# Performance work log

Measured on AMD Instinct MI355X. Metric: run time of the kernel, lower is better.

## Reference

```python
import jax, jax.numpy as jnp
import numpy as np

L = 401            # cfg.n_anchor_bins
MIN_SEP = 2        # cfg.min_separation_bins
TARGET_ALPHA = 0.85
DIST_W, CTCF_W, COMP_W = 1.0, 0.5, 0.5
RATIO_TARGET = 1.5


def setup_inputs() -> dict:
    key = jax.random.key(0)
    k1, k2, k3 = jax.random.split(key, 3)
    B = 256
    contact_map = jax.random.normal(k1, (B, L, L), dtype=jnp.float32)
    compartment_logits = jax.random.normal(k2, (B, L, 2), dtype=jnp.float32)
    ctcf_orientation = (jax.random.randint(k3, (B, L), 0, 3) - 1).astype(jnp.int32)  # {-1,0,1}
    return {"contact_map": contact_map,
            "compartment_logits": compartment_logits,
            "ctcf_orientation": ctcf_orientation}


def reference(contact_map, compartment_logits, ctcf_orientation):
    B, Ld, _ = contact_map.shape
    dt = contact_map.dtype
    idx = jnp.arange(Ld)
    d = jnp.abs(idx[:, None] - idx[None, :])          # (L, L) int distance bins

    # ---- distance decay loss: one segment-reduce instead of a loop over bins ----
    bins = d.reshape(-1)                               # (L*L,)
    cm_sum = contact_map.sum(0).reshape(-1)            # sum over batch, flattened
    per_bin_sum = jax.ops.segment_sum(cm_sum, bins, num_segments=Ld)
    counts = jax.ops.segment_sum(jnp.ones_like(cm_sum), bins, num_segments=Ld)
    mean_c = per_bin_sum / (counts * B)                # mean contact per distance s
    s_vals = jnp.arange(Ld).astype(dt)
    valid = (idx >= MIN_SEP) & jnp.isfinite(mean_c) & (mean_c > 0)
    w = valid.astype(dt)
    n = w.sum()
    log_d = jnp.log(jnp.maximum(s_vals, 1.0))
    log_p = jnp.log(jnp.where(valid, mean_c, 1.0) + 1e-6)
    n_safe = jnp.maximum(n, 1.0)
    x_mean = (w * log_d).sum() / n_safe
    y_mean = (w * log_p).sum() / n_safe
    num = (w * (log_d - x_mean) * (log_p - y_mean)).sum()
    den = (w * (log_d - x_mean) ** 2).sum() + 1e-8
    slope = num / den
    dist_loss = jnp.where(n >= 5, (slope + TARGET_ALPHA) ** 2, jnp.zeros((), dt))

    # ---- CTCF convergence loss ----
    f = (ctcf_orientation == 1).astype(dt)             # (B, L)
    r = (ctcf_orientation == -1).astype(dt)
    convergent = f[:, :, None] * r[:, None, :]         # (B, L, L)
    any_c = (ctcf_orientation != 0).astype(dt)
    any_pair = any_c[:, :, None] * any_c[:, None, :]
    non_conv = any_pair * (1.0 - convergent)
    nc_sum = non_conv.sum()
    hinge = (jax.nn.relu(contact_map) * non_conv).sum() / (nc_sum + 1e-6)
    ctcf_loss = jnp.where(nc_sum < 1.0, jnp.zeros((), dt), hinge)

    # ---- compartment loss ----
    comp = jnp.argmax(jax.lax.stop_gradient(compartment_logits), axis=-1)  # (B, L)
    same = (comp[:, :, None] == comp[:, None, :]).astype(dt)               # (B, L, L)
    maskf = (d >= MIN_SEP).astype(dt)[None]                                # (1, L, L)
    within = (contact_map * same * maskf).sum() / jnp.maximum((same * maskf).sum(), 1.0)
    between = (contact_map * (1.0 - same) * maskf).sum() / jnp.maximum(((1.0 - same) * maskf).sum(), 1.0)
    ratio = within / (jnp.abs(between) + 1e-6)
    comp_loss = jax.nn.relu(RATIO_TARGET - ratio)

    total = DIST_W * dist_loss + CTCF_W * ctcf_loss + COMP_W * comp_loss
    return jnp.stack([dist_loss, ctcf_loss, comp_loss, total])
```

## Files before the change

kernel.cpp:

```cpp
#include <hip/hip_runtime.h>
#include <cmath>

#define LBINS 401
#define LL 160801
#define MIN_SEP 2
#define PSTRIDE 405
#define UNR 8

#define ACC_HANY  401
#define ACC_HCONV 402
#define ACC_SWM   403
#define ACC_SMM   404

__global__ __launch_bounds__(256)
void main_kernel(const float* __restrict__ cm,
                 const float* __restrict__ logits,
                 const int* __restrict__ ctcf,
                 float* __restrict__ parts,
                 int* __restrict__ partsI,
                 int* __restrict__ cnt) {
    int b      = blockIdx.x;
    int B      = gridDim.x;
    int ihalf  = blockIdx.y & 1;
    int kgroup = blockIdx.y >> 1;
    int u      = threadIdx.x;
    int k      = kgroup * 256 + u;
    bool active = (k < LBINS);

    __shared__ unsigned char colx8[LBINS];
    __shared__ __align__(8) unsigned char row8[LBINS + 7];
    __shared__ float lb[LBINS];
    __shared__ float sred[4][4];
    __shared__ int   ired[4][4];

    const int*   ct = ctcf   + (size_t)b * LBINS;
    const float* lg = logits + (size_t)b * LBINS * 2;
    for (int t = u; t < LBINS; t += 256) {
        int o = ct[t];
        unsigned any = (o != 0)  ? 1u : 0u;
        unsigned rev = (o == -1) ? 1u : 0u;
        unsigned fwd = (o == 1)  ? 1u : 0u;
        unsigned cj  = (lg[2 * t + 1] > lg[2 * t]) ? 1u : 0u;
        colx8[t] = (unsigned char)(any | (rev << 1) | (cj << 2));
        row8[t]  = (unsigned char)(any | (fwd << 1) | ((1u - cj) << 2));
        lb[t] = 0.f;
    }
    if (u < 7) row8[LBINS + u] = 0;
    if (b == 0 && blockIdx.y == 0 && u == 0)
        __hip_atomic_store(cnt, 0, __ATOMIC_RELAXED, __HIP_MEMORY_SCOPE_AGENT);
    __syncthreads();

    if (blockIdx.y == 0) {
        int na = 0, nr = 0, n1 = 0, adj = 0;
        for (int t = u; t < LBINS; t += 256) {
            unsigned cb = colx8[t];
            na += (int)(cb & 1u);
            nr += (int)((cb >> 1) & 1u);
            n1 += (int)((cb >> 2) & 1u);
            if (t >= 1) adj += (int)((((cb ^ colx8[t - 1]) >> 2) & 1u) ^ 1u);
        }
        #pragma unroll
        for (int off = 32; off > 0; off >>= 1) {
            na  += __shfl_down(na,  off, 64);
            nr  += __shfl_down(nr,  off, 64);
            n1  += __shfl_down(n1,  off, 64);
            adj += __shfl_down(adj, off, 64);
        }
        int w = u >> 6;
        if ((u & 63) == 0) {
            ired[w][0] = na; ired[w][1] = nr; ired[w][2] = n1; ired[w][3] = adj;
        }
        __syncthreads();
        if (u == 0) {
            int NA = ired[0][0] + ired[1][0] + ired[2][0] + ired[3][0];
            int NR = ired[0][1] + ired[1][1] + ired[2][1] + ired[3][1];
            int N1 = ired[0][2] + ired[1][2] + ired[2][2] + ired[3][2];
            int AD = ired[0][3] + ired[1][3] + ired[2][3] + ired[3][3];
            int NF = NA - NR;
            int N0 = LBINS - N1;
            partsI[b]     = NA * NA - NF * NR;
            partsI[B + b] = N0 * N0 + N1 * N1 - LBINS - 2 * AD;
        }
    }

    int i0 = ihalf ? 201 : 0;
    int ie = ihalf ? LBINS : 201;

    const float* cmb = cm + (size_t)b * LL;
    float HA = 0.f, HC = 0.f;
    float SMk = 0.f, SMw = 0.f, SWk = 0.f, SWw = 0.f;

    if (active) {
        auto scalar_step = [&](int ii) {
            int j = ii + k;
            int wrapped = (j >= LBINS);
            int jc = wrapped ? j - LBINS : j;
            float c = cmb[(size_t)ii * LBINS + jc];
            unsigned cbq = colx8[jc];
            unsigned rbq = row8[ii];
            float rc = fmaxf(c, 0.f);
            unsigned bnd = rbq & cbq;
            int m0 = (int)(bnd << 31) >> 31;
            int m1 = (int)(bnd << 30) >> 31;
            int ms = (int)((rbq ^ cbq) << 29) >> 31;
            HA += __int_as_float(__float_as_int(rc) & m0);
            HC += __int_as_float(__float_as_int(rc) & m1);
            float cs = __int_as_float(__float_as_int(c) & ms);
            SMw += wrapped ? c   : 0.f;
            SMk += wrapped ? 0.f : c;
            SWw += wrapped ? cs  : 0.f;
            SWk += wrapped ? 0.f : cs;
        };

        int i  = i0;
        int iu = i0 + ((8 - (i0 & 7)) & 7);
        if (iu > ie) iu = ie;
        for (; i < iu; ++i) scalar_step(i);
        for (; i + UNR <= ie; i += UNR) {
            unsigned long long rwin = *(const unsigned long long*)(row8 + i);
            float    cv[UNR];
            unsigned cb[UNR];
            int      wr[UNR];
            #pragma unroll
            for (int q = 0; q < UNR; ++q) {
                int ii = i + q;
                int j  = ii + k;
                int wrapped = (j >= LBINS);
                int jc = wrapped ? j - LBINS : j;
                cv[q] = cmb[(size_t)ii * LBINS + jc];
                cb[q] = colx8[jc];
                wr[q] = wrapped;
            }
            #pragma unroll
            for (int q = 0; q < UNR; ++q) {
                unsigned rbq = (unsigned)(rwin >> (8 * q)) & 0xffu;
                float c  = cv[q];
                float rc = fmaxf(c, 0.f);
                unsigned bnd = rbq & cb[q];
                int m0 = (int)(bnd << 31) >> 31;
                int m1 = (int)(bnd << 30) >> 31;
                int ms = (int)((rbq ^ cb[q]) << 29) >> 31;
                HA += __int_as_float(__float_as_int(rc) & m0);
                HC += __int_as_float(__float_as_int(rc) & m1);
                float cs = __int_as_float(__float_as_int(c) & ms);
                SMw += wr[q] ? c   : 0.f;
                SMk += wr[q] ? 0.f : c;
                SWw += wr[q] ? cs  : 0.f;
                SWk += wr[q] ? 0.f : cs;
            }
        }
        for (; i < ie; ++i) scalar_step(i);
    }

    float SWm = 0.f, SMm = 0.f;
    if (active) {
        int dw = LBINS - k;
        atomicAdd(&lb[k], SMk);
        if (k > 0) atomicAdd(&lb[dw], SMw);
        float mk = (k  >= MIN_SEP) ? 1.f : 0.f;
        float mw = (dw >= MIN_SEP) ? 1.f : 0.f;
        SWm = SWk * mk + SWw * mw;
        SMm = SMk * mk + SMw * mw;
    }

    #pragma unroll
    for (int off = 32; off > 0; off >>= 1) {
        HA  += __shfl_down(HA,  off, 64);
        HC  += __shfl_down(HC,  off, 64);
        SWm += __shfl_down(SWm, off, 64);
        SMm += __shfl_down(SMm, off, 64);
    }
    int w = u >> 6;
    if ((u & 63) == 0) {
        sred[w][0] = HA; sred[w][1] = HC; sred[w][2] = SWm; sred[w][3] = SMm;
    }
    __syncthreads();

    float* pout = parts + (size_t)(blockIdx.y * gridDim.x + blockIdx.x) * PSTRIDE;
    for (int t = u; t < LBINS; t += 256) pout[t] = lb[t];
    if (u == 0) {
        float a = 0.f, c2 = 0.f, s = 0.f, m = 0.f;
        #pragma unroll
        for (int q = 0; q < 4; ++q) {
            a += sred[q][0]; c2 += sred[q][1]; s += sred[q][2]; m += sred[q][3];
        }
        pout[ACC_HANY] = a; pout[ACC_HCONV] = c2;
        pout[ACC_SWM]  = s; pout[ACC_SMM]   = m;
    }
}

__device__ double br256(double v, double* buf) {
    int tid = threadIdx.x;
    buf[tid] = v;
    __syncthreads();
    for (int off = 128; off > 0; off >>= 1) {
        if (tid < off) buf[tid] += buf[tid + off];
        __syncthreads();
    }
    double r = buf[0];
    __syncthreads();
    return r;
}

__global__ __launch_bounds__(256)
void reduce_final_kernel(const float* __restrict__ parts,
                         const int* __restrict__ partsI,
                         float* __restrict__ accum,
                         int* __restrict__ accumI,
                         int* __restrict__ cnt,
                         float* __restrict__ out,
                         int B) {
    int s = blockIdx.x;
    int u = threadIdx.x;
    int npart = 4 * B;
    __shared__ float r4[4];
    __shared__ int   ri4[4];
    __shared__ int   lastFlag;

    if (s < PSTRIDE) {
        float acc = 0.f;
        for (int p = u; p < npart; p += 256) acc += parts[(size_t)p * PSTRIDE + s];
        #pragma unroll
        for (int off = 32; off > 0; off >>= 1) acc += __shfl_down(acc, off, 64);
        if ((u & 63) == 0) r4[u >> 6] = acc;
        __syncthreads();
        if (u == 0)
            __hip_atomic_store(&accum[s], r4[0] + r4[1] + r4[2] + r4[3],
                               __ATOMIC_RELAXED, __HIP_MEMORY_SCOPE_AGENT);
    } else {
        int col = s - PSTRIDE;
        int acc = 0;
        for (int p = u; p < B; p += 256) acc += partsI[col * B + p];
        #pragma unroll
        for (int off = 32; off > 0; off >>= 1) acc += __shfl_down(acc, off, 64);
        if ((u & 63) == 0) ri4[u >> 6] = acc;
        __syncthreads();
        if (u == 0)
            __hip_atomic_store(&accumI[col], ri4[0] + ri4[1] + ri4[2] + ri4[3],
                               __ATOMIC_RELAXED, __HIP_MEMORY_SCOPE_AGENT);
    }

    if (u == 0) {
        int prev = __hip_atomic_fetch_add(cnt, 1, __ATOMIC_ACQ_REL,
                                          __HIP_MEMORY_SCOPE_AGENT);
        lastFlag = (prev == (int)gridDim.x - 1);
    }
    __syncthreads();
    if (!lastFlag) return;

    __shared__ double dred[256];

    double nc_sum   = (double)__hip_atomic_load(&accumI[0], __ATOMIC_RELAXED,
                                                __HIP_MEMORY_SCOPE_AGENT);
    double same_cnt = (double)__hip_atomic_load(&accumI[1], __ATOMIC_RELAXED,
                                                __HIP_MEMORY_SCOPE_AGENT);
    double total_maskf = (double)B * ((double)LL - 3.0 * LBINS + 2.0);
    double diff_cnt = total_maskf - same_cnt;

    float w0 = 0.f, x0 = 0.f, y0 = 0.f;
    float w1 = 0.f, x1 = 0.f, y1 = 0.f;
    {
        int t0 = u;
        float a0 = __hip_atomic_load(&accum[t0], __ATOMIC_RELAXED,
                                     __HIP_MEMORY_SCOPE_AGENT);
        float cntB = ((t0 == 0) ? (float)LBINS : 2.0f * (float)(LBINS - t0)) * (float)B;
        float mc = a0 / cntB;
        int valid = (t0 >= MIN_SEP) && __builtin_isfinite(mc) && (mc > 0.0f);
        w0 = valid ? 1.f : 0.f;
        x0 = logf(fmaxf((float)t0, 1.0f));
        y0 = logf((valid ? mc : 1.0f) + 1e-6f);
    }
    int t1 = u + 256;
    if (t1 < LBINS) {
        float a1 = __hip_atomic_load(&accum[t1], __ATOMIC_RELAXED,
                                     __HIP_MEMORY_SCOPE_AGENT);
        float cntB = 2.0f * (float)(LBINS - t1) * (float)B;
        float mc = a1 / cntB;
        int valid = __builtin_isfinite(mc) && (mc > 0.0f);
        w1 = valid ? 1.f : 0.f;
        x1 = logf((float)t1);
        y1 = logf((valid ? mc : 1.0f) + 1e-6f);
    }
    double n  = br256((double)w0 + (double)w1, dred);
    double Sx = br256((double)(w0 * x0) + (double)(w1 * x1), dred);
    double Sy = br256((double)(w0 * y0) + (double)(w1 * y1), dred);
    double n_safe = fmax(n, 1.0);
    double xm = Sx / n_safe, ym = Sy / n_safe;
    double num = br256((double)w0 * ((double)x0 - xm) * ((double)y0 - ym)
                     + (double)w1 * ((double)x1 - xm) * ((double)y1 - ym), dred);
    double den = br256((double)w0 * ((double)x0 - xm) * ((double)x0 - xm)
                     + (double)w1 * ((double)x1 - xm) * ((double)x1 - xm), dred);

    if (u == 0) {
        double slope = num / (den + 1e-8);
        float dist_loss = (n >= 5.0) ? (float)((slope + 0.85) * (slope + 0.85)) : 0.0f;

        float fHA = __hip_atomic_load(&accum[ACC_HANY],  __ATOMIC_RELAXED, __HIP_MEMORY_SCOPE_AGENT);
        float fHC = __hip_atomic_load(&accum[ACC_HCONV], __ATOMIC_RELAXED, __HIP_MEMORY_SCOPE_AGENT);
        float fSW = __hip_atomic_load(&accum[ACC_SWM],   __ATOMIC_RELAXED, __HIP_MEMORY_SCOPE_AGENT);
        float fSM = __hip_atomic_load(&accum[ACC_SMM],   __ATOMIC_RELAXED, __HIP_MEMORY_SCOPE_AGENT);

        float ncf = (float)nc_sum;
        float hinge = (fHA - fHC) / (ncf + 1e-6f);
        float ctcf_loss = (ncf < 1.0f) ? 0.0f : hinge;

        float within  = fSW / (float)fmax(same_cnt, 1.0);
        float between = (fSM - fSW) / (float)fmax(diff_cnt, 1.0);
        float ratio = within / (fabsf(between) + 1e-6f);
        float comp_loss = fmaxf(1.5f - ratio, 0.0f);

        float total = 1.0f * dist_loss + 0.5f * ctcf_loss + 0.5f * comp_loss;
        out[0] = dist_loss;
        out[1] = ctcf_loss;
        out[2] = comp_loss;
        out[3] = total;
    }
}

extern "C" void kernel_launch(void* const* d_in, const int* in_sizes, int n_in,
                              void* d_out, int out_size, void* d_ws, size_t ws_size,
                              hipStream_t stream) {
    const float* cm     = (const float*)d_in[0];
    const float* logits = (const float*)d_in[1];
    const int*   ctcf   = (const int*)d_in[2];
    float* out = (float*)d_out;

    int total = in_sizes[0];
    int B = total / LL;

    float* wsf    = (float*)d_ws;
    float* accum  = wsf;
    int*   accumI = (int*)(wsf + 408);
    int*   cnt    = (int*)(wsf + 412);
    int*   partsI = (int*)(wsf + 416);
    int parts_off = (416 + 2 * B + 255) & ~255;
    float* parts  = wsf + parts_off;

    main_kernel<<<dim3(B, 4), 256, 0, stream>>>(cm, logits, ctcf, parts, partsI, cnt);
    reduce_final_kernel<<<PSTRIDE + 2, 256, 0, stream>>>(parts, partsI, accum,
                                                         accumI, cnt, out, B);
}
```

Measured before the change: 253.9 us.

## Split rows into three segments and double-buffer unrolled loads in main kernel

```diff
diff --git a/kernel.cpp b/kernel.cpp
--- a/kernel.cpp
+++ b/kernel.cpp
@@ -6,13 +6,15 @@
 #define MIN_SEP 2
 #define PSTRIDE 405
 #define UNR 8
+#define NSEG 3
+#define NYB  (NSEG * 2)
 
 #define ACC_HANY  401
 #define ACC_HCONV 402
 #define ACC_SWM   403
 #define ACC_SMM   404
 
-__global__ __launch_bounds__(256)
+__global__ __launch_bounds__(256, 6)
 void main_kernel(const float* __restrict__ cm,
                  const float* __restrict__ logits,
                  const int* __restrict__ ctcf,
@@ -21,13 +23,14 @@
                  int* __restrict__ cnt) {
     int b      = blockIdx.x;
     int B      = gridDim.x;
-    int ihalf  = blockIdx.y & 1;
-    int kgroup = blockIdx.y >> 1;
+    int y      = blockIdx.y;
+    int iseg   = y >> 1;
+    int kgroup = y & 1;
     int u      = threadIdx.x;
     int k      = kgroup * 256 + u;
     bool active = (k < LBINS);
 
-    __shared__ unsigned char colx8[LBINS];
+    __shared__ unsigned int colu[LBINS];
     __shared__ __align__(8) unsigned char row8[LBINS + 7];
     __shared__ float lb[LBINS];
     __shared__ float sred[4][4];
@@ -41,23 +44,23 @@
         unsigned rev = (o == -1) ? 1u : 0u;
         unsigned fwd = (o == 1)  ? 1u : 0u;
         unsigned cj  = (lg[2 * t + 1] > lg[2 * t]) ? 1u : 0u;
-        colx8[t] = (unsigned char)(any | (rev << 1) | (cj << 2));
-        row8[t]  = (unsigned char)(any | (fwd << 1) | ((1u - cj) << 2));
+        colu[t] = any | (rev << 1) | (cj << 2);
+        row8[t] = (unsigned char)(any | (fwd << 1) | ((1u - cj) << 2));
         lb[t] = 0.f;
     }
     if (u < 7) row8[LBINS + u] = 0;
-    if (b == 0 && blockIdx.y == 0 && u == 0)
+    if (b == 0 && y == 0 && u == 0)
         __hip_atomic_store(cnt, 0, __ATOMIC_RELAXED, __HIP_MEMORY_SCOPE_AGENT);
     __syncthreads();
 
-    if (blockIdx.y == 0) {
+    if (y == 0) {
         int na = 0, nr = 0, n1 = 0, adj = 0;
         for (int t = u; t < LBINS; t += 256) {
-            unsigned cb = colx8[t];
+            unsigned cb = colu[t];
             na += (int)(cb & 1u);
             nr += (int)((cb >> 1) & 1u);
             n1 += (int)((cb >> 2) & 1u);
-            if (t >= 1) adj += (int)((((cb ^ colx8[t - 1]) >> 2) & 1u) ^ 1u);
+            if (t >= 1) adj += (int)((((cb ^ colu[t - 1]) >> 2) & 1u) ^ 1u);
         }
         #pragma unroll
         for (int off = 32; off > 0; off >>= 1) {
@@ -83,73 +86,113 @@
         }
     }
 
-    int i0 = ihalf ? 201 : 0;
-    int ie = ihalf ? LBINS : 201;
+    int i0 = (iseg == 0) ? 0   : (iseg == 1) ? 134 : 268;
+    int ie = (iseg == 0) ? 134 : (iseg == 1) ? 268 : 401;
 
     const float* cmb = cm + (size_t)b * LL;
     float HA = 0.f, HC = 0.f;
     float SMk = 0.f, SMw = 0.f, SWk = 0.f, SWw = 0.f;
 
     if (active) {
-        auto scalar_step = [&](int ii) {
-            int j = ii + k;
-            int wrapped = (j >= LBINS);
-            int jc = wrapped ? j - LBINS : j;
-            float c = cmb[(size_t)ii * LBINS + jc];
-            unsigned cbq = colx8[jc];
-            unsigned rbq = row8[ii];
-            float rc = fmaxf(c, 0.f);
-            unsigned bnd = rbq & cbq;
-            int m0 = (int)(bnd << 31) >> 31;
-            int m1 = (int)(bnd << 30) >> 31;
-            int ms = (int)((rbq ^ cbq) << 29) >> 31;
-            HA += __int_as_float(__float_as_int(rc) & m0);
-            HC += __int_as_float(__float_as_int(rc) & m1);
-            float cs = __int_as_float(__float_as_int(c) & ms);
-            SMw += wrapped ? c   : 0.f;
-            SMk += wrapped ? 0.f : c;
-            SWw += wrapped ? cs  : 0.f;
-            SWk += wrapped ? 0.f : cs;
-        };
+        int wthr = LBINS - k;
+
+#define STEP1(II)                                                          \
+    do {                                                                   \
+        int ii_ = (II);                                                    \
+        int j_ = ii_ + k;                                                  \
+        bool wr_ = (j_ >= LBINS);                                          \
+        int jc_ = wr_ ? j_ - LBINS : j_;                                   \
+        float c_ = cmb[(unsigned)(ii_ * LBINS + jc_)];                     \
+        unsigned cbq_ = colu[jc_];                                         \
+        unsigned rbq_ = row8[ii_];                                         \
+        float rc_ = fmaxf(c_, 0.f);                                        \
+        unsigned bnd_ = rbq_ & cbq_;                                       \
+        int m0_ = (int)(bnd_ << 31) >> 31;                                 \
+        int m1_ = (int)(bnd_ << 30) >> 31;                                 \
+        int ms_ = (int)((rbq_ ^ cbq_) << 29) >> 31;                        \
+        HA += __int_as_float(__float_as_int(rc_) & m0_);                   \
+        HC += __int_as_float(__float_as_int(rc_) & m1_);                   \
+        float cs_ = __int_as_float(__float_as_int(c_) & ms_);              \
+        float ct_  = wr_ ? c_  : 0.f;                                      \
+        float cst_ = wr_ ? cs_ : 0.f;                                      \
+        SMw += ct_;  SMk += (c_ - ct_);                                    \
+        SWw += cst_; SWk += (cs_ - cst_);                                  \
+    } while (0)
+
+#define PRE(IB, CV, CB, RW)                                                \
+    do {                                                                   \
+        int ib_ = (IB);                                                    \
+        RW = *(const unsigned long long*)(row8 + ib_);                     \
+        _Pragma("unroll")                                                  \
+        for (int q = 0; q < UNR; ++q) {                                    \
+            int ii_ = ib_ + q;                                             \
+            int j_ = ii_ + k;                                              \
+            int jc_ = (j_ >= LBINS) ? j_ - LBINS : j_;                     \
+            CV[q] = cmb[(unsigned)(ii_ * LBINS + jc_)];                    \
+            CB[q] = colu[jc_];                                             \
+        }                                                                  \
+    } while (0)
+
+#define CMP(IB, CV, CB, RW)                                                \
+    do {                                                                   \
+        int ib_ = (IB);                                                    \
+        _Pragma("unroll")                                                  \
+        for (int q = 0; q < UNR; ++q) {                                    \
+            unsigned cbq_ = CB[q];                                         \
+            unsigned rbq_ = (unsigned)((RW) >> (8 * q)) & 0xffu;           \
+            float c_ = CV[q];                                              \
+            bool wr_ = (ib_ + q) >= wthr;                                  \
+            float rc_ = fmaxf(c_, 0.f);                                    \
+            unsigned bnd_ = rbq_ & cbq_;                                   \
+            int m0_ = (int)(bnd_ << 31) >> 31;                             \
+            int m1_ = (int)(bnd_ << 30) >> 31;                             \
+            int ms_ = (int)((rbq_ ^ cbq_) << 29) >> 31;                    \
+            HA += __int_as_float(__float_as_int(rc_) & m0_);               \
+            HC += __int_as_float(__float_as_int(rc_) & m1_);               \
+            float cs_ = __int_as_float(__float_as_int(c_) & ms_);          \
+            float ct_  = wr_ ? c_  : 0.f;                                  \
+            float cst_ = wr_ ? cs_ : 0.f;                                  \
+            SMw += ct_;  SMk += (c_ - ct_);                                \
+            SWw += cst_; SWk += (cs_ - cst_);                              \
+        }                                                                  \
+    } while (0)
 
         int i  = i0;
         int iu = i0 + ((8 - (i0 & 7)) & 7);
         if (iu > ie) iu = ie;
-        for (; i < iu; ++i) scalar_step(i);
-        for (; i + UNR <= ie; i += UNR) {
-            unsigned long long rwin = *(const unsigned long long*)(row8 + i);
-            float    cv[UNR];
-            unsigned cb[UNR];
-            int      wr[UNR];
-            #pragma unroll
-            for (int q = 0; q < UNR; ++q) {
-                int ii = i + q;
-                int j  = ii + k;
-                int wrapped = (j >= LBINS);
-                int jc = wrapped ? j - LBINS : j;
-                cv[q] = cmb[(size_t)ii * LBINS + jc];
-                cb[q] = colx8[jc];
-                wr[q] = wrapped;
+        for (; i < iu; ++i) STEP1(i);
+
+        int nb = (ie - i) >> 3;
+        if (nb > 0) {
+            float cvA[UNR], cvB[UNR];
+            unsigned cbA[UNR], cbB[UNR];
+            unsigned long long rwA, rwB;
+            int ibA = i, ibB;
+
+            PRE(ibA, cvA, cbA, rwA);
+            i += 8; --nb;
+            while (nb >= 2) {
+                ibB = i; PRE(ibB, cvB, cbB, rwB);
+                CMP(ibA, cvA, cbA, rwA);
+                i += 8;
+                ibA = i; PRE(ibA, cvA, cbA, rwA);
+                CMP(ibB, cvB, cbB, rwB);
+                i += 8;
+                nb -= 2;
             }
-            #pragma unroll
-            for (int q = 0; q < UNR; ++q) {
-                unsigned rbq = (unsigned)(rwin >> (8 * q)) & 0xffu;
-                float c  = cv[q];
-                float rc = fmaxf(c, 0.f);
-                unsigned bnd = rbq & cb[q];
-                int m0 = (int)(bnd << 31) >> 31;
-                int m1 = (int)(bnd << 30) >> 31;
-                int ms = (int)((rbq ^ cb[q]) << 29) >> 31;
-                HA += __int_as_float(__float_as_int(rc) & m0);
-                HC += __int_as_float(__float_as_int(rc) & m1);
-                float cs = __int_as_float(__float_as_int(c) & ms);
-                SMw += wr[q] ? c   : 0.f;
-                SMk += wr[q] ? 0.f : c;
-                SWw += wr[q] ? cs  : 0.f;
-                SWk += wr[q] ? 0.f : cs;
+            if (nb == 1) {
+                ibB = i; PRE(ibB, cvB, cbB, rwB);
+                CMP(ibA, cvA, cbA, rwA);
+                i += 8;
+                CMP(ibB, cvB, cbB, rwB);
+            } else {
+                CMP(ibA, cvA, cbA, rwA);
             }
         }
-        for (; i < ie; ++i) scalar_step(i);
+        for (; i < ie; ++i) STEP1(i);
+#undef STEP1
+#undef PRE
+#undef CMP
     }
 
     float SWm = 0.f, SMm = 0.f;
@@ -176,7 +219,7 @@
     }
     __syncthreads();
 
-    float* pout = parts + (size_t)(blockIdx.y * gridDim.x + blockIdx.x) * PSTRIDE;
+    float* pout = parts + (size_t)(y * gridDim.x + b) * PSTRIDE;
     for (int t = u; t < LBINS; t += 256) pout[t] = lb[t];
     if (u == 0) {
         float a = 0.f, c2 = 0.f, s = 0.f, m = 0.f;
@@ -212,7 +255,7 @@
                          int B) {
     int s = blockIdx.x;
     int u = threadIdx.x;
-    int npart = 4 * B;
+    int npart = NYB * B;
     __shared__ float r4[4];
     __shared__ int   ri4[4];
     __shared__ int   lastFlag;
@@ -336,7 +379,7 @@
     int parts_off = (416 + 2 * B + 255) & ~255;
     float* parts  = wsf + parts_off;
 
-    main_kernel<<<dim3(B, 4), 256, 0, stream>>>(cm, logits, ctcf, parts, partsI, cnt);
+    main_kernel<<<dim3(B, NYB), 256, 0, stream>>>(cm, logits, ctcf, parts, partsI, cnt);
     reduce_final_kernel<<<PSTRIDE + 2, 256, 0, stream>>>(parts, partsI, accum,
                                                          accumI, cnt, out, B);
 }
```

After: 256.6 us. Within noise of the previous version (+1.1%).

## Use 512-thread blocks over all diagonals with three row segments per batch

Applied to the files above, without the earlier changes.

```diff
diff --git a/kernel.cpp b/kernel.cpp
--- a/kernel.cpp
+++ b/kernel.cpp
@@ -6,58 +6,59 @@
 #define MIN_SEP 2
 #define PSTRIDE 405
 #define UNR 8
+#define NSEG 3
+#define BLK 512
 
 #define ACC_HANY  401
 #define ACC_HCONV 402
 #define ACC_SWM   403
 #define ACC_SMM   404
 
-__global__ __launch_bounds__(256)
+__global__ __launch_bounds__(BLK, 6)
 void main_kernel(const float* __restrict__ cm,
                  const float* __restrict__ logits,
                  const int* __restrict__ ctcf,
                  float* __restrict__ parts,
                  int* __restrict__ partsI,
                  int* __restrict__ cnt) {
-    int b      = blockIdx.x;
-    int B      = gridDim.x;
-    int ihalf  = blockIdx.y & 1;
-    int kgroup = blockIdx.y >> 1;
-    int u      = threadIdx.x;
-    int k      = kgroup * 256 + u;
+    int b    = blockIdx.x;
+    int B    = gridDim.x;
+    int iseg = blockIdx.y;
+    int u    = threadIdx.x;
+    int k    = u;
     bool active = (k < LBINS);
 
-    __shared__ unsigned char colx8[LBINS];
+    __shared__ unsigned int colu[LBINS];
     __shared__ __align__(8) unsigned char row8[LBINS + 7];
     __shared__ float lb[LBINS];
-    __shared__ float sred[4][4];
-    __shared__ int   ired[4][4];
+    __shared__ float sred[8][4];
+    __shared__ int   ired[8][4];
 
     const int*   ct = ctcf   + (size_t)b * LBINS;
     const float* lg = logits + (size_t)b * LBINS * 2;
-    for (int t = u; t < LBINS; t += 256) {
+    for (int t = u; t < LBINS; t += BLK) {
         int o = ct[t];
         unsigned any = (o != 0)  ? 1u : 0u;
         unsigned rev = (o == -1) ? 1u : 0u;
         unsigned fwd = (o == 1)  ? 1u : 0u;
         unsigned cj  = (lg[2 * t + 1] > lg[2 * t]) ? 1u : 0u;
-        colx8[t] = (unsigned char)(any | (rev << 1) | (cj << 2));
-        row8[t]  = (unsigned char)(any | (fwd << 1) | ((1u - cj) << 2));
+        colu[t] = any | (rev << 1) | (cj << 2);
+        row8[t] = (unsigned char)(any | (fwd << 1) | ((1u - cj) << 2));
         lb[t] = 0.f;
     }
     if (u < 7) row8[LBINS + u] = 0;
-    if (b == 0 && blockIdx.y == 0 && u == 0)
+    if (b == 0 && iseg == 0 && u == 0)
         __hip_atomic_store(cnt, 0, __ATOMIC_RELAXED, __HIP_MEMORY_SCOPE_AGENT);
     __syncthreads();
 
-    if (blockIdx.y == 0) {
+    if (iseg == 0) {
         int na = 0, nr = 0, n1 = 0, adj = 0;
-        for (int t = u; t < LBINS; t += 256) {
-            unsigned cb = colx8[t];
+        for (int t = u; t < LBINS; t += BLK) {
+            unsigned cb = colu[t];
             na += (int)(cb & 1u);
             nr += (int)((cb >> 1) & 1u);
             n1 += (int)((cb >> 2) & 1u);
-            if (t >= 1) adj += (int)((((cb ^ colx8[t - 1]) >> 2) & 1u) ^ 1u);
+            if (t >= 1) adj += (int)((((cb ^ colu[t - 1]) >> 2) & 1u) ^ 1u);
         }
         #pragma unroll
         for (int off = 32; off > 0; off >>= 1) {
@@ -72,10 +73,12 @@
         }
         __syncthreads();
         if (u == 0) {
-            int NA = ired[0][0] + ired[1][0] + ired[2][0] + ired[3][0];
-            int NR = ired[0][1] + ired[1][1] + ired[2][1] + ired[3][1];
-            int N1 = ired[0][2] + ired[1][2] + ired[2][2] + ired[3][2];
-            int AD = ired[0][3] + ired[1][3] + ired[2][3] + ired[3][3];
+            int NA = 0, NR = 0, N1 = 0, AD = 0;
+            #pragma unroll
+            for (int q = 0; q < 8; ++q) {
+                NA += ired[q][0]; NR += ired[q][1];
+                N1 += ired[q][2]; AD += ired[q][3];
+            }
             int NF = NA - NR;
             int N0 = LBINS - N1;
             partsI[b]     = NA * NA - NF * NR;
@@ -83,8 +86,8 @@
         }
     }
 
-    int i0 = ihalf ? 201 : 0;
-    int ie = ihalf ? LBINS : 201;
+    int i0 = (iseg == 0) ? 0   : (iseg == 1) ? 134 : 268;
+    int ie = (iseg == 0) ? 134 : (iseg == 1) ? 268 : 401;
 
     const float* cmb = cm + (size_t)b * LL;
     float HA = 0.f, HC = 0.f;
@@ -93,10 +96,10 @@
     if (active) {
         auto scalar_step = [&](int ii) {
             int j = ii + k;
-            int wrapped = (j >= LBINS);
-            int jc = wrapped ? j - LBINS : j;
-            float c = cmb[(size_t)ii * LBINS + jc];
-            unsigned cbq = colx8[jc];
+            bool wr = (j >= LBINS);
+            int jc = wr ? j - LBINS : j;
+            float c = cmb[(unsigned)(ii * LBINS + jc)];
+            unsigned cbq = colu[jc];
             unsigned rbq = row8[ii];
             float rc = fmaxf(c, 0.f);
             unsigned bnd = rbq & cbq;
@@ -106,10 +109,10 @@
             HA += __int_as_float(__float_as_int(rc) & m0);
             HC += __int_as_float(__float_as_int(rc) & m1);
             float cs = __int_as_float(__float_as_int(c) & ms);
-            SMw += wrapped ? c   : 0.f;
-            SMk += wrapped ? 0.f : c;
-            SWw += wrapped ? cs  : 0.f;
-            SWk += wrapped ? 0.f : cs;
+            float ctv = wr ? c  : 0.f;
+            float cst = wr ? cs : 0.f;
+            SMw += ctv;  SMk += (c - ctv);
+            SWw += cst;  SWk += (cs - cst);
         };
 
         int i  = i0;
@@ -120,16 +123,16 @@
             unsigned long long rwin = *(const unsigned long long*)(row8 + i);
             float    cv[UNR];
             unsigned cb[UNR];
-            int      wr[UNR];
+            int      wrv[UNR];
             #pragma unroll
             for (int q = 0; q < UNR; ++q) {
                 int ii = i + q;
                 int j  = ii + k;
-                int wrapped = (j >= LBINS);
-                int jc = wrapped ? j - LBINS : j;
-                cv[q] = cmb[(size_t)ii * LBINS + jc];
-                cb[q] = colx8[jc];
-                wr[q] = wrapped;
+                int wr = (j >= LBINS);
+                int jc = wr ? j - LBINS : j;
+                cv[q]  = cmb[(unsigned)(ii * LBINS + jc)];
+                cb[q]  = colu[jc];
+                wrv[q] = wr;
             }
             #pragma unroll
             for (int q = 0; q < UNR; ++q) {
@@ -143,10 +146,10 @@
                 HA += __int_as_float(__float_as_int(rc) & m0);
                 HC += __int_as_float(__float_as_int(rc) & m1);
                 float cs = __int_as_float(__float_as_int(c) & ms);
-                SMw += wr[q] ? c   : 0.f;
-                SMk += wr[q] ? 0.f : c;
-                SWw += wr[q] ? cs  : 0.f;
-                SWk += wr[q] ? 0.f : cs;
+                float ctv = wrv[q] ? c  : 0.f;
+                float cst = wrv[q] ? cs : 0.f;
+                SMw += ctv;  SMk += (c - ctv);
+                SWw += cst;  SWk += (cs - cst);
             }
         }
         for (; i < ie; ++i) scalar_step(i);
@@ -176,12 +179,12 @@
     }
     __syncthreads();
 
-    float* pout = parts + (size_t)(blockIdx.y * gridDim.x + blockIdx.x) * PSTRIDE;
-    for (int t = u; t < LBINS; t += 256) pout[t] = lb[t];
+    float* pout = parts + (size_t)(iseg * gridDim.x + b) * PSTRIDE;
+    for (int t = u; t < LBINS; t += BLK) pout[t] = lb[t];
     if (u == 0) {
         float a = 0.f, c2 = 0.f, s = 0.f, m = 0.f;
         #pragma unroll
-        for (int q = 0; q < 4; ++q) {
+        for (int q = 0; q < 8; ++q) {
             a += sred[q][0]; c2 += sred[q][1]; s += sred[q][2]; m += sred[q][3];
         }
         pout[ACC_HANY] = a; pout[ACC_HCONV] = c2;
@@ -212,7 +215,7 @@
                          int B) {
     int s = blockIdx.x;
     int u = threadIdx.x;
-    int npart = 4 * B;
+    int npart = NSEG * B;
     __shared__ float r4[4];
     __shared__ int   ri4[4];
     __shared__ int   lastFlag;
@@ -336,7 +339,7 @@
     int parts_off = (416 + 2 * B + 255) & ~255;
     float* parts  = wsf + parts_off;
 
-    main_kernel<<<dim3(B, 4), 256, 0, stream>>>(cm, logits, ctcf, parts, partsI, cnt);
+    main_kernel<<<dim3(B, NSEG), BLK, 0, stream>>>(cm, logits, ctcf, parts, partsI, cnt);
     reduce_final_kernel<<<PSTRIDE + 2, 256, 0, stream>>>(parts, partsI, accum,
                                                          accumI, cnt, out, B);
 }
```

Result: no change. 255.6 us (+0.6%).
